# Performance work log

Measured on AMD Instinct MI355X. Metric: run time of the kernel, lower is better.

The kernel has to match this reference:

```python
import jax, jax.numpy as jnp
import numpy as np

B, N, D, H = 2, 2048, 1024, 16
Dh = D // H
SCALE = Dh ** -0.5


def setup_inputs() -> dict:
    key = jax.random.key(0)
    ks = jax.random.split(key, 5)
    init = lambda k, sh, fan: (jax.random.normal(k, sh, jnp.float32) / np.sqrt(fan)).astype(jnp.float32)
    return {
        "x": jax.random.normal(ks[0], (B, N, D), jnp.float32),
        "w_qkv": init(ks[1], (D, 3 * D), D),   # to_qkv (no bias)
        "w_hkv": init(ks[2], (D, 2 * D), D),   # hkv_processor: Linear(dim, 2*dim), split -> HK, HV
        "w_out": init(ks[3], (D, D), D),       # to_out weight
        "b_out": jnp.zeros((D,), jnp.float32), # to_out bias
        "alpha": jnp.ones((1, H, 1, 1), jnp.float32),
    }


def _split_heads(t):  # (B,N,D) -> (B,H,N,Dh)
    return t.reshape(B, N, H, Dh).transpose(0, 2, 1, 3)


def _rope(x, theta=10000.0):
    # lucidrains rotary_embedding_torch: interleaved pairs (x[2i], x[2i+1])
    n, dh = x.shape[-2], x.shape[-1]
    freqs = 1.0 / (theta ** (jnp.arange(0, dh, 2, dtype=jnp.float32) / dh))
    ang = jnp.arange(n, dtype=jnp.float32)[:, None] * freqs          # (N, Dh/2)
    cos = jnp.repeat(jnp.cos(ang), 2, axis=-1)                        # (N, Dh)
    sin = jnp.repeat(jnp.sin(ang), 2, axis=-1)
    xp = x.reshape(*x.shape[:-1], dh // 2, 2)
    xrot = jnp.stack((-xp[..., 1], xp[..., 0]), axis=-1).reshape(x.shape)
    return x * cos + xrot * sin


def reference(x, w_qkv, w_hkv, w_out, b_out, alpha):
    q, k, v = (_split_heads(t) for t in jnp.split(x @ w_qkv, 3, axis=-1))
    hk, hv = (_split_heads(t) for t in jnp.split(x @ w_hkv, 2, axis=-1))
    q = _rope(q)
    k = _rope(k)

    qk = jnp.einsum('bhnd,bhmd->bhnm', q, k) * SCALE          # (B,H,N,N)
    hkk = jnp.einsum('bhnd,bhmd->bhnm', hk, k)                # (B,H,N,N)
    qhk = jnp.sum(q * hk, axis=-1, keepdims=True)             # (B,H,N,1)
    scores = qk - jax.nn.silu(hkk * qhk * SCALE)

    mask = jnp.tril(jnp.ones((N, N), dtype=bool))
    scores = jnp.where(mask, scores, -jnp.inf)
    W = jax.nn.softmax(scores, axis=-1)

    hvv = jnp.einsum('bhnd,bhmd->bhnm', hv, v)                # (B,H,N,N)
    mod = jnp.sum(hvv * W, axis=-1, keepdims=True)            # (B,H,N,1)
    o = jnp.einsum('bhnm,bhmd->bhnd', W, v) - jax.nn.sigmoid(alpha) * mod * hv

    attn_out = o.transpose(0, 2, 1, 3).reshape(B, N, D)
    return attn_out @ w_out + b_out
```

## Files before the change

kernel.cpp:

```cpp
#include <hip/hip_runtime.h>
#include <math.h>

typedef unsigned int u32;
typedef unsigned short u16;
typedef __attribute__((ext_vector_type(4))) float f32x4;
typedef __attribute__((ext_vector_type(8))) short s16x8;

#define BB 2
#define NN 2048
#define DD 1024
#define HH 16
#define ROWS 4096
#define QC 5120
#define SCALE 0.125f
#define LOG2E 1.44269504088896f
#define SC2 (SCALE * LOG2E)

#if __has_builtin(__builtin_amdgcn_exp2f)
#define EXP2(x) __builtin_amdgcn_exp2f(x)
#else
#define EXP2(x) __expf((x) * 0.69314718056f)
#endif
#if __has_builtin(__builtin_amdgcn_rcpf)
#define RCP(x) __builtin_amdgcn_rcpf(x)
#else
#define RCP(x) (1.0f / (x))
#endif

__device__ __forceinline__ u16 f2bf(float x) {
    u32 u = __float_as_uint(x);
    return (u16)((u + 0x7FFFu + ((u >> 16) & 1u)) >> 16);
}
__device__ __forceinline__ float bf2f(u16 h) {
    return __uint_as_float(((u32)h) << 16);
}
__device__ __forceinline__ u32 cvtpk(float lo, float hi) {
    u32 r;
    asm("v_cvt_pk_bf16_f32 %0, %1, %2" : "=v"(r) : "v"(lo), "v"(hi));
    return r;
}
__device__ __forceinline__ void gload16(const void* g, void* l) {
    __builtin_amdgcn_global_load_lds(
        (const __attribute__((address_space(1))) unsigned int*)g,
        (__attribute__((address_space(3))) unsigned int*)l, 16, 0, 0);
}

__device__ __forceinline__ void vt_write(char* vbb, uint4 vreg, int srow, int sch)
{
    uint4 oth;
    oth.x = (u32)__shfl_xor((int)vreg.x, 8); oth.y = (u32)__shfl_xor((int)vreg.y, 8);
    oth.z = (u32)__shfl_xor((int)vreg.z, 8); oth.w = (u32)__shfl_xor((int)vreg.w, 8);
    const bool odd = (srow & 1);
    u32 ma = odd ? vreg.z : vreg.x, mb = odd ? vreg.w : vreg.y;
    u32 oa = odd ? oth.z : oth.x,  ob = odd ? oth.w : oth.y;
    u32 ea = odd ? oa : ma, eb = odd ? ob : mb;
    u32 da = odd ? ma : oa, db = odd ? mb : ob;
    u32 pk0 = (ea & 0xffffu) | (da << 16);
    u32 pk1 = (ea >> 16)     | (da & 0xffff0000u);
    u32 pk2 = (eb & 0xffffu) | (db << 16);
    u32 pk3 = (eb >> 16)     | (db & 0xffff0000u);
    const int s = srow >> 1;
    const int d0 = sch * 8 + (odd ? 4 : 0);
    *(u32*)(vbb + (d0 + 0) * 128 + ((((s >> 2) ^ ((d0 + 0) & 7)) << 4)) + (s & 3) * 4) = pk0;
    *(u32*)(vbb + (d0 + 1) * 128 + ((((s >> 2) ^ ((d0 + 1) & 7)) << 4)) + (s & 3) * 4) = pk1;
    *(u32*)(vbb + (d0 + 2) * 128 + ((((s >> 2) ^ ((d0 + 2) & 7)) << 4)) + (s & 3) * 4) = pk2;
    *(u32*)(vbb + (d0 + 3) * 128 + ((((s >> 2) ^ ((d0 + 3) & 7)) << 4)) + (s & 3) * 4) = pk3;
}

__global__ __launch_bounds__(256) void convert_x(const float* __restrict__ x,
                                                 uint4* __restrict__ xb)
{
    int t = blockIdx.x * 256 + threadIdx.x;
    const float4 a = ((const float4*)x)[2 * t];
    const float4 b = ((const float4*)x)[2 * t + 1];
    uint4 o;
    o.x = f2bf(a.x) | ((u32)f2bf(a.y) << 16);
    o.y = f2bf(a.z) | ((u32)f2bf(a.w) << 16);
    o.z = f2bf(b.x) | ((u32)f2bf(b.y) << 16);
    o.w = f2bf(b.z) | ((u32)f2bf(b.w) << 16);
    xb[t] = o;
}

__global__ __launch_bounds__(256) void transpose_w(const float* __restrict__ wqkv,
                                                   const float* __restrict__ whkv,
                                                   const float* __restrict__ wout,
                                                   u16* __restrict__ wT)
{
    __shared__ float T[64][65];
    const int bc = blockIdx.x;
    const int k0 = blockIdx.y * 64;
    const int c0 = bc * 64;
    const float* src; int stride; int csrc;
    if (bc < 48)      { src = wqkv; stride = 3072; csrc = c0; }
    else if (bc < 80) { src = whkv; stride = 2048; csrc = c0 - 3072; }
    else              { src = wout; stride = 1024; csrc = c0 - 5120; }
    const int t = threadIdx.x;
    const int r = t >> 4, c4 = t & 15;
#pragma unroll
    for (int i = 0; i < 4; ++i) {
        int kk = r + 16 * i;
        float4 v = *(const float4*)&src[(size_t)(k0 + kk) * stride + csrc + 4 * c4];
        T[kk][4 * c4 + 0] = v.x; T[kk][4 * c4 + 1] = v.y;
        T[kk][4 * c4 + 2] = v.z; T[kk][4 * c4 + 3] = v.w;
    }
    __syncthreads();
#pragma unroll
    for (int i = 0; i < 4; ++i) {
        int cc = r + 16 * i;
        u32 lo = f2bf(T[4 * c4 + 0][cc]) | ((u32)f2bf(T[4 * c4 + 1][cc]) << 16);
        u32 hi = f2bf(T[4 * c4 + 2][cc]) | ((u32)f2bf(T[4 * c4 + 3][cc]) << 16);
        *(uint2*)&wT[(size_t)(c0 + cc) * 1024 + k0 + 4 * c4] = make_uint2(lo, hi);
    }
}

__global__ __launch_bounds__(256) void rope_table(float* __restrict__ tab)
{
    int t = blockIdx.x * 256 + threadIdx.x;
    int n = t >> 6, col = t & 63, i = col & 31;
    float ang = (float)n * exp2f(-(float)i * 0.41524101186092029f);
    tab[t] = (col < 32) ? cosf(ang) : sinf(ang);
}

template <int BF16_OUT>
__global__ __launch_bounds__(256, 2) void gemm_bf16(
    const u16* __restrict__ A, int lda,
    const u16* __restrict__ B, int ldb,
    void* __restrict__ C, int ldc,
    const float* __restrict__ bias, const float* __restrict__ tab, int K)
{
    __shared__ u16 As[128 * 64];
    __shared__ u16 Bs[128 * 64];
    const int tid = threadIdx.x;
    const int lane = tid & 63, w = tid >> 6;
    const int g = lane >> 4, c = lane & 15;
    const int wr = w >> 1, wc = w & 1;
    const int rb0 = blockIdx.y * 128, cb0 = blockIdx.x * 128;

    f32x4 acc[4][4];
#pragma unroll
    for (int i = 0; i < 4; ++i)
#pragma unroll
        for (int j = 0; j < 4; ++j) {
            acc[i][j][0] = 0.f; acc[i][j][1] = 0.f; acc[i][j][2] = 0.f; acc[i][j][3] = 0.f;
        }

    const int srow = tid >> 3, sch = tid & 7;
    const int scol = ((sch ^ (srow & 7)) * 8);
    const u16* asrc = A + (size_t)(rb0 + srow) * lda + scol;
    const u16* bsrc = B + (size_t)(cb0 + srow) * ldb + scol;

    for (int k0 = 0; k0 < K; k0 += 64) {
        __syncthreads();
#pragma unroll
        for (int r = 0; r < 4; ++r) {
            gload16(asrc + (size_t)(32 * r) * lda + k0, (char*)As + r * 4096 + w * 1024);
            gload16(bsrc + (size_t)(32 * r) * ldb + k0, (char*)Bs + r * 4096 + w * 1024);
        }
        __syncthreads();
#pragma unroll
        for (int kk = 0; kk < 2; ++kk) {
            s16x8 a[4], b[4];
#pragma unroll
            for (int rb = 0; rb < 4; ++rb) {
                int row = wr * 64 + rb * 16 + c;
                a[rb] = *(const s16x8*)((const char*)As + row * 128 + ((((kk << 2) + g) ^ (row & 7)) << 4));
            }
#pragma unroll
            for (int cb = 0; cb < 4; ++cb) {
                int row = wc * 64 + cb * 16 + c;
                b[cb] = *(const s16x8*)((const char*)Bs + row * 128 + ((((kk << 2) + g) ^ (row & 7)) << 4));
            }
#pragma unroll
            for (int rb = 0; rb < 4; ++rb)
#pragma unroll
                for (int cb = 0; cb < 4; ++cb)
                    acc[rb][cb] = __builtin_amdgcn_mfma_f32_16x16x32_bf16(a[rb], b[cb], acc[rb][cb], 0, 0, 0);
        }
    }

    if (BF16_OUT && tab && cb0 >= 1024 && cb0 < 2048) {
#pragma unroll
        for (int rb = 0; rb < 4; ++rb)
#pragma unroll
            for (int cb = 0; cb < 4; ++cb) {
                const int i = ((wc * 64 + cb * 16 + c) & 63) >> 1;
#pragma unroll
                for (int e = 0; e < 4; ++e) {
                    int n = (rb0 + wr * 64 + rb * 16 + g * 4 + e) & (NN - 1);
                    float co = tab[(n << 6) + i], si = tab[(n << 6) + 32 + i];
                    float self = acc[rb][cb][e];
                    float part = __shfl_xor(self, 1);
                    acc[rb][cb][e] = (c & 1) ? fmaf(self, co, part * si)
                                             : fmaf(self, co, -part * si);
                }
            }
    }

#pragma unroll
    for (int rb = 0; rb < 4; ++rb) {
#pragma unroll
        for (int cb = 0; cb < 4; ++cb) {
            if (BF16_OUT) {
                uint2 keep = make_uint2(0, 0);
#pragma unroll
                for (int e = 0; e < 4; ++e) {
                    u32 me = f2bf(acc[rb][cb][e]);
                    u32 x1 = (u32)__shfl_xor((int)me, 1);
                    u32 pair = (c & 1) ? ((x1 & 0xffffu) | (me << 16)) : ((me & 0xffffu) | (x1 << 16));
                    u32 x2 = (u32)__shfl_xor((int)pair, 2);
                    u32 q0 = (c & 2) ? x2 : pair;
                    u32 q1 = (c & 2) ? pair : x2;
                    if ((c & 3) == e) keep = make_uint2(q0, q1);
                }
                int row = rb0 + wr * 64 + rb * 16 + g * 4 + (c & 3);
                int col = cb0 + wc * 64 + cb * 16 + (c & ~3);
                *(uint2*)((u16*)C + (size_t)row * ldc + col) = keep;
            } else {
                int col = cb0 + wc * 64 + cb * 16 + c;
                float bv = bias ? bias[col] : 0.f;
#pragma unroll
                for (int e = 0; e < 4; ++e) {
                    int row = rb0 + wr * 64 + rb * 16 + g * 4 + e;
                    ((float*)C)[(size_t)row * ldc + col] = acc[rb][cb][e] + bv;
                }
            }
        }
    }
}

__global__ __launch_bounds__(256, 4) void attn(
    const u16* __restrict__ qkvh, const float* __restrict__ alpha,
    const float* __restrict__ tab, u16* __restrict__ aout)
{
    __shared__ u16 Kb[2][64 * 64];
    __shared__ u16 Vt[2][64 * 64];

    const int bid = blockIdx.x;
    const int swz = (bid & 7) * 64 + (bid >> 3);
    const int bh = swz >> 4;
    const int qp = swz & 15;
    const int b = bh >> 4, h = bh & 15;
    const int tid = threadIdx.x;
    const int w = tid >> 6, lane = tid & 63;
    const int g = lane >> 4, c = lane & 15;
    const u16* base = qkvh + (size_t)b * NN * QC;

    const int srow = tid >> 3, sch = tid & 7;
    const int kscol = (sch ^ ((srow & 3) | (((srow >> 3) & 1) << 2))) * 8;
    const u16* ksrc0 = base + (size_t)srow * QC + 1024 + h * 64 + kscol;
    const u16* vsrc0 = base + (size_t)srow * QC + 2048 + h * 64 + sch * 8;

    const float sig_a = RCP(1.f + EXP2(-alpha[h] * LOG2E));
    const int cbase = (8 * (c >> 2) + (c & 3)) * 128;

#pragma unroll 1
    for (int ph = 0; ph < 2; ++ph) {
        const int qt = ph ? (31 - qp) : qp;
        const int q0 = qt * 64;
        const int nrow = q0 + w * 16 + c;

        gload16(ksrc0 + (size_t)(q0 - q0) , (char*)&Kb[0][0] + w * 1024);
        gload16(ksrc0 + (size_t)32 * QC, (char*)&Kb[0][0] + 4096 + w * 1024);
        uint4 vr0 = *(const uint4*)vsrc0;
        uint4 vr1 = *(const uint4*)(vsrc0 + (size_t)32 * QC);
        vt_write((char*)&Vt[0][0], vr0, srow, sch);
        vt_write((char*)&Vt[0][0], vr1, srow + 32, sch);

        s16x8 qf[2], hf[2];
        float qhL;
        {
            const u16* qp_ = base + (size_t)nrow * QC + h * 64;
            float accq = 0.f;
#pragma unroll
            for (int kk = 0; kk < 2; ++kk) {
                uint4 qv = *(const uint4*)(qp_ + ((kk * 4 + g) * 8));
                uint4 hv = *(const uint4*)(qp_ + 3072 + ((kk * 4 + g) * 8));
                const u16* qe = (const u16*)&qv;
                const u16* he = (const u16*)&hv;
                u32 ow[4];
#pragma unroll
                for (int m2 = 0; m2 < 4; ++m2) {
                    int i = (kk * 4 + g) * 4 + m2;
                    float co = tab[(nrow << 6) + i], si = tab[(nrow << 6) + 32 + i];
                    float x0 = bf2f(qe[2 * m2]), x1 = bf2f(qe[2 * m2 + 1]);
                    float r0 = x0 * co - x1 * si;
                    float r1 = x1 * co + x0 * si;
                    accq += r0 * bf2f(he[2 * m2]) + r1 * bf2f(he[2 * m2 + 1]);
                    ow[m2] = (u32)f2bf(r0) | ((u32)f2bf(r1) << 16);
                }
                union { s16x8 v; u32 u[4]; } uq, uh;
                uq.u[0] = ow[0]; uq.u[1] = ow[1]; uq.u[2] = ow[2]; uq.u[3] = ow[3];
                uh.u[0] = hv.x; uh.u[1] = hv.y; uh.u[2] = hv.z; uh.u[3] = hv.w;
                qf[kk] = uq.v; hf[kk] = uh.v;
            }
            accq += __shfl_xor(accq, 16);
            accq += __shfl_xor(accq, 32);
            qhL = accq * SC2;
        }
        __syncthreads();

        f32x4 y[4];
#pragma unroll
        for (int db = 0; db < 4; ++db) { y[db][0] = 0.f; y[db][1] = 0.f; y[db][2] = 0.f; y[db][3] = 0.f; }
        float m = -INFINITY, l = 0.f;

        for (int kt = 0; kt <= qt; ++kt) {
            const int cur = kt & 1;
            const bool haveNext = (kt < qt);
            uint4 vr0n, vr1n;
            if (haveNext) {
                gload16(ksrc0 + (size_t)((kt + 1) * 64) * QC, (char*)&Kb[cur ^ 1][0] + w * 1024);
                gload16(ksrc0 + (size_t)((kt + 1) * 64 + 32) * QC, (char*)&Kb[cur ^ 1][0] + 4096 + w * 1024);
                vr0n = *(const uint4*)(vsrc0 + (size_t)((kt + 1) * 64) * QC);
                vr1n = *(const uint4*)(vsrc0 + (size_t)((kt + 1) * 64 + 32) * QC);
            }

            f32x4 sq[4], sh4[4];
#pragma unroll
            for (int kb = 0; kb < 4; ++kb) {
                sq[kb][0] = 0.f; sq[kb][1] = 0.f; sq[kb][2] = 0.f; sq[kb][3] = 0.f;
                sh4[kb][0] = 0.f; sh4[kb][1] = 0.f; sh4[kb][2] = 0.f; sh4[kb][3] = 0.f;
            }
            const char* kbp = (const char*)&Kb[cur][0] + cbase;
#pragma unroll
            for (int kb = 0; kb < 4; ++kb) {
#pragma unroll
                for (int kk = 0; kk < 2; ++kk) {
                    s16x8 kf = *(const s16x8*)(kbp + (kb & 1) * 512 + (kb >> 1) * 4096 +
                                               ((((kk << 2) + g) ^ (c & 7)) << 4));
                    sq[kb] = __builtin_amdgcn_mfma_f32_16x16x32_bf16(kf, qf[kk], sq[kb], 0, 0, 0);
                    sh4[kb] = __builtin_amdgcn_mfma_f32_16x16x32_bf16(kf, hf[kk], sh4[kb], 0, 0, 0);
                }
            }
            const bool needmask = (kt == qt);
            float mx = -INFINITY;
#pragma unroll
            for (int kb = 0; kb < 4; ++kb) {
#pragma unroll
                for (int e = 0; e < 4; ++e) {
                    float zp = sh4[kb][e] * qhL;
                    float sil = zp * RCP(1.f + EXP2(-zp));
                    float s = fmaf(sq[kb][e], SC2, -sil);
                    if (needmask) {
                        int kg = kt * 64 + 32 * (kb >> 1) + 8 * g + 4 * (kb & 1) + e;
                        if (kg > nrow) s = -INFINITY;
                    }
                    sq[kb][e] = s;
                    mx = fmaxf(mx, s);
                }
            }
            mx = fmaxf(mx, __shfl_xor(mx, 16));
            mx = fmaxf(mx, __shfl_xor(mx, 32));
            const float mnew = fmaxf(m, mx);
            const float scl = EXP2(m - mnew);
            m = mnew;
            float rs = 0.f;
#pragma unroll
            for (int kb = 0; kb < 4; ++kb)
#pragma unroll
                for (int e = 0; e < 4; ++e) {
                    float p = EXP2(sq[kb][e] - mnew);
                    sq[kb][e] = p;
                    rs += p;
                }
            rs += __shfl_xor(rs, 16);
            rs += __shfl_xor(rs, 32);
            l = l * scl + rs;
#pragma unroll
            for (int db = 0; db < 4; ++db) {
                y[db][0] *= scl; y[db][1] *= scl; y[db][2] *= scl; y[db][3] *= scl;
            }
            union { s16x8 v; u32 u[4]; } pa[2];
#pragma unroll
            for (int kk = 0; kk < 2; ++kk) {
                pa[kk].u[0] = cvtpk(sq[2 * kk][0], sq[2 * kk][1]);
                pa[kk].u[1] = cvtpk(sq[2 * kk][2], sq[2 * kk][3]);
                pa[kk].u[2] = cvtpk(sq[2 * kk + 1][0], sq[2 * kk + 1][1]);
                pa[kk].u[3] = cvtpk(sq[2 * kk + 1][2], sq[2 * kk + 1][3]);
            }
            const char* vbp = (const char*)&Vt[cur][0];
#pragma unroll
            for (int kk = 0; kk < 2; ++kk)
#pragma unroll
                for (int db = 0; db < 4; ++db) {
                    int row = db * 16 + c;
                    s16x8 vfr = *(const s16x8*)(vbp + row * 128 + ((((kk << 2) + g) ^ (c & 7)) << 4));
                    y[db] = __builtin_amdgcn_mfma_f32_16x16x32_bf16(vfr, pa[kk].v, y[db], 0, 0, 0);
                }

            if (haveNext) {
                vt_write((char*)&Vt[cur ^ 1][0], vr0n, srow, sch);
                vt_write((char*)&Vt[cur ^ 1][0], vr1n, srow + 32, sch);
            }
            __syncthreads();
        }

        const float inv_l = RCP(l);
        const u16* hvp = base + (size_t)nrow * QC + 4096 + h * 64 + g * 4;
        float hv[4][4];
        float sdot = 0.f;
#pragma unroll
        for (int db = 0; db < 4; ++db) {
            uint2 hw = *(const uint2*)(hvp + db * 16);
            const u16* he = (const u16*)&hw;
#pragma unroll
            for (int e = 0; e < 4; ++e) {
                hv[db][e] = bf2f(he[e]);
                float yn = y[db][e] * inv_l;
                y[db][e] = yn;
                sdot += yn * hv[db][e];
            }
        }
        sdot += __shfl_xor(sdot, 1); sdot += __shfl_xor(sdot, 2);
        sdot += __shfl_xor(sdot, 4); sdot += __shfl_xor(sdot, 8);
        sdot = 0.f;
#pragma unroll
        for (int db = 0; db < 4; ++db)
#pragma unroll
            for (int e = 0; e < 4; ++e) sdot += y[db][e] * hv[db][e];
        sdot += __shfl_xor(sdot, 16);
        sdot += __shfl_xor(sdot, 32);
        const float f = sig_a * sdot;
        u16* op = aout + ((size_t)(b * NN + nrow)) * DD + h * 64 + g * 4;
#pragma unroll
        for (int db = 0; db < 4; ++db) {
            u32 o0 = (u32)f2bf(y[db][0] - f * hv[db][0]) | ((u32)f2bf(y[db][1] - f * hv[db][1]) << 16);
            u32 o1 = (u32)f2bf(y[db][2] - f * hv[db][2]) | ((u32)f2bf(y[db][3] - f * hv[db][3]) << 16);
            *(uint2*)(op + db * 16) = make_uint2(o0, o1);
        }
        __syncthreads();
    }
}

extern "C" void kernel_launch(void* const* d_in, const int* in_sizes, int n_in,
                              void* d_out, int out_size, void* d_ws, size_t ws_size,
                              hipStream_t stream)
{
    const float* x     = (const float*)d_in[0];
    const float* w_qkv = (const float*)d_in[1];
    const float* w_hkv = (const float*)d_in[2];
    const float* w_out = (const float*)d_in[3];
    const float* b_out = (const float*)d_in[4];
    const float* alpha = (const float*)d_in[5];

    char* ws = (char*)d_ws;
    u16*   qkvh = (u16*)ws;
    uint4* xb   = (uint4*)(ws + 41943040);
    u16*   wT   = (u16*)(ws + 50331648);
    u16*   aout = (u16*)(ws + 62914560);
    float* tab  = (float*)(ws + 71303168);

    convert_x<<<2048, 256, 0, stream>>>(x, xb);
    transpose_w<<<dim3(96, 16), 256, 0, stream>>>(w_qkv, w_hkv, w_out, wT);
    rope_table<<<512, 256, 0, stream>>>(tab);

    gemm_bf16<1><<<dim3(40, 32), 256, 0, stream>>>(
        (const u16*)xb, 1024, wT, 1024, qkvh, QC, nullptr, tab, 1024);

    attn<<<512, 256, 0, stream>>>(qkvh, alpha, tab, aout);

    gemm_bf16<0><<<dim3(8, 32), 256, 0, stream>>>(
        aout, 1024, wT + 5120 * 1024, 1024, d_out, 1024, b_out, nullptr, 1024);
}
```

Before: 183.8 us.

## Split paired causal tiles into separate blocks and add V-transpose LDS swizzle

Each attention block used to process a pair of q-tiles (qp and 31-qp) to balance causal work. Now it processes a single q-tile, and the grid doubles to 1024 blocks ordered longest-first so the scheduler can balance the load dynamically. The Vt shared-memory layout gains an extra XOR swizzle term, applied both where it is written and where it is read, to reduce bank conflicts. The change also removes a dead shuffle reduction. The risk is a tail of short blocks and repeated per-block setup.

```diff
diff --git a/kernel.cpp b/kernel.cpp
--- a/kernel.cpp
+++ b/kernel.cpp
@@ -61,10 +61,11 @@
     u32 pk3 = (eb >> 16)     | (db & 0xffff0000u);
     const int s = srow >> 1;
     const int d0 = sch * 8 + (odd ? 4 : 0);
-    *(u32*)(vbb + (d0 + 0) * 128 + ((((s >> 2) ^ ((d0 + 0) & 7)) << 4)) + (s & 3) * 4) = pk0;
-    *(u32*)(vbb + (d0 + 1) * 128 + ((((s >> 2) ^ ((d0 + 1) & 7)) << 4)) + (s & 3) * 4) = pk1;
-    *(u32*)(vbb + (d0 + 2) * 128 + ((((s >> 2) ^ ((d0 + 2) & 7)) << 4)) + (s & 3) * 4) = pk2;
-    *(u32*)(vbb + (d0 + 3) * 128 + ((((s >> 2) ^ ((d0 + 3) & 7)) << 4)) + (s & 3) * 4) = pk3;
+    const int sb = (s & 3) * 4;
+    *(u32*)(vbb + (d0 + 0) * 128 + ((((s >> 2) ^ ((d0 + 0) & 7) ^ sch) << 4)) + sb) = pk0;
+    *(u32*)(vbb + (d0 + 1) * 128 + ((((s >> 2) ^ ((d0 + 1) & 7) ^ sch) << 4)) + sb) = pk1;
+    *(u32*)(vbb + (d0 + 2) * 128 + ((((s >> 2) ^ ((d0 + 2) & 7) ^ sch) << 4)) + sb) = pk2;
+    *(u32*)(vbb + (d0 + 3) * 128 + ((((s >> 2) ^ ((d0 + 3) & 7) ^ sch) << 4)) + sb) = pk3;
 }
 
 __global__ __launch_bounds__(256) void convert_x(const float* __restrict__ x,
@@ -236,14 +237,15 @@
     __shared__ u16 Vt[2][64 * 64];
 
     const int bid = blockIdx.x;
-    const int swz = (bid & 7) * 64 + (bid >> 3);
-    const int bh = swz >> 4;
-    const int qp = swz & 15;
+    const int qt = 31 - (bid >> 5);
+    const int bh = 4 * (bid & 7) + ((bid >> 3) & 3);
     const int b = bh >> 4, h = bh & 15;
     const int tid = threadIdx.x;
     const int w = tid >> 6, lane = tid & 63;
     const int g = lane >> 4, c = lane & 15;
     const u16* base = qkvh + (size_t)b * NN * QC;
+    const int q0 = qt * 64;
+    const int nrow = q0 + w * 16 + c;
 
     const int srow = tid >> 3, sch = tid & 7;
     const int kscol = (sch ^ ((srow & 3) | (((srow >> 3) & 1) << 2))) * 8;
@@ -253,182 +255,168 @@
     const float sig_a = RCP(1.f + EXP2(-alpha[h] * LOG2E));
     const int cbase = (8 * (c >> 2) + (c & 3)) * 128;
 
-#pragma unroll 1
-    for (int ph = 0; ph < 2; ++ph) {
-        const int qt = ph ? (31 - qp) : qp;
-        const int q0 = qt * 64;
-        const int nrow = q0 + w * 16 + c;
-
-        gload16(ksrc0 + (size_t)(q0 - q0) , (char*)&Kb[0][0] + w * 1024);
-        gload16(ksrc0 + (size_t)32 * QC, (char*)&Kb[0][0] + 4096 + w * 1024);
-        uint4 vr0 = *(const uint4*)vsrc0;
-        uint4 vr1 = *(const uint4*)(vsrc0 + (size_t)32 * QC);
-        vt_write((char*)&Vt[0][0], vr0, srow, sch);
-        vt_write((char*)&Vt[0][0], vr1, srow + 32, sch);
-
-        s16x8 qf[2], hf[2];
-        float qhL;
-        {
-            const u16* qp_ = base + (size_t)nrow * QC + h * 64;
-            float accq = 0.f;
+    gload16(ksrc0, (char*)&Kb[0][0] + w * 1024);
+    gload16(ksrc0 + (size_t)32 * QC, (char*)&Kb[0][0] + 4096 + w * 1024);
+    uint4 vr0 = *(const uint4*)vsrc0;
+    uint4 vr1 = *(const uint4*)(vsrc0 + (size_t)32 * QC);
+    vt_write((char*)&Vt[0][0], vr0, srow, sch);
+    vt_write((char*)&Vt[0][0], vr1, srow + 32, sch);
+
+    s16x8 qf[2], hf[2];
+    float qhL;
+    {
+        const u16* qp_ = base + (size_t)nrow * QC + h * 64;
+        float accq = 0.f;
+#pragma unroll
+        for (int kk = 0; kk < 2; ++kk) {
+            uint4 qv = *(const uint4*)(qp_ + ((kk * 4 + g) * 8));
+            uint4 hv = *(const uint4*)(qp_ + 3072 + ((kk * 4 + g) * 8));
+            const u16* qe = (const u16*)&qv;
+            const u16* he = (const u16*)&hv;
+            u32 ow[4];
+#pragma unroll
+            for (int m2 = 0; m2 < 4; ++m2) {
+                int i = (kk * 4 + g) * 4 + m2;
+                float co = tab[(nrow << 6) + i], si = tab[(nrow << 6) + 32 + i];
+                float x0 = bf2f(qe[2 * m2]), x1 = bf2f(qe[2 * m2 + 1]);
+                float r0 = x0 * co - x1 * si;
+                float r1 = x1 * co + x0 * si;
+                accq += r0 * bf2f(he[2 * m2]) + r1 * bf2f(he[2 * m2 + 1]);
+                ow[m2] = (u32)f2bf(r0) | ((u32)f2bf(r1) << 16);
+            }
+            union { s16x8 v; u32 u[4]; } uq, uh;
+            uq.u[0] = ow[0]; uq.u[1] = ow[1]; uq.u[2] = ow[2]; uq.u[3] = ow[3];
+            uh.u[0] = hv.x; uh.u[1] = hv.y; uh.u[2] = hv.z; uh.u[3] = hv.w;
+            qf[kk] = uq.v; hf[kk] = uh.v;
+        }
+        accq += __shfl_xor(accq, 16);
+        accq += __shfl_xor(accq, 32);
+        qhL = accq * SC2;
+    }
+    __syncthreads();
+
+    f32x4 y[4];
+#pragma unroll
+    for (int db = 0; db < 4; ++db) { y[db][0] = 0.f; y[db][1] = 0.f; y[db][2] = 0.f; y[db][3] = 0.f; }
+    float m = -INFINITY, l = 0.f;
+
+    for (int kt = 0; kt <= qt; ++kt) {
+        const int cur = kt & 1;
+        const bool haveNext = (kt < qt);
+        uint4 vr0n, vr1n;
+        if (haveNext) {
+            gload16(ksrc0 + (size_t)((kt + 1) * 64) * QC, (char*)&Kb[cur ^ 1][0] + w * 1024);
+            gload16(ksrc0 + (size_t)((kt + 1) * 64 + 32) * QC, (char*)&Kb[cur ^ 1][0] + 4096 + w * 1024);
+            vr0n = *(const uint4*)(vsrc0 + (size_t)((kt + 1) * 64) * QC);
+            vr1n = *(const uint4*)(vsrc0 + (size_t)((kt + 1) * 64 + 32) * QC);
+        }
+
+        f32x4 sq[4], sh4[4];
+#pragma unroll
+        for (int kb = 0; kb < 4; ++kb) {
+            sq[kb][0] = 0.f; sq[kb][1] = 0.f; sq[kb][2] = 0.f; sq[kb][3] = 0.f;
+            sh4[kb][0] = 0.f; sh4[kb][1] = 0.f; sh4[kb][2] = 0.f; sh4[kb][3] = 0.f;
+        }
+        const char* kbp = (const char*)&Kb[cur][0] + cbase;
+#pragma unroll
+        for (int kb = 0; kb < 4; ++kb) {
 #pragma unroll
             for (int kk = 0; kk < 2; ++kk) {
-                uint4 qv = *(const uint4*)(qp_ + ((kk * 4 + g) * 8));
-                uint4 hv = *(const uint4*)(qp_ + 3072 + ((kk * 4 + g) * 8));
-                const u16* qe = (const u16*)&qv;
-                const u16* he = (const u16*)&hv;
-                u32 ow[4];
-#pragma unroll
-                for (int m2 = 0; m2 < 4; ++m2) {
-                    int i = (kk * 4 + g) * 4 + m2;
-                    float co = tab[(nrow << 6) + i], si = tab[(nrow << 6) + 32 + i];
-                    float x0 = bf2f(qe[2 * m2]), x1 = bf2f(qe[2 * m2 + 1]);
-                    float r0 = x0 * co - x1 * si;
-                    float r1 = x1 * co + x0 * si;
-                    accq += r0 * bf2f(he[2 * m2]) + r1 * bf2f(he[2 * m2 + 1]);
-                    ow[m2] = (u32)f2bf(r0) | ((u32)f2bf(r1) << 16);
+                s16x8 kf = *(const s16x8*)(kbp + (kb & 1) * 512 + (kb >> 1) * 4096 +
+                                           ((((kk << 2) + g) ^ (c & 7)) << 4));
+                sq[kb] = __builtin_amdgcn_mfma_f32_16x16x32_bf16(kf, qf[kk], sq[kb], 0, 0, 0);
+                sh4[kb] = __builtin_amdgcn_mfma_f32_16x16x32_bf16(kf, hf[kk], sh4[kb], 0, 0, 0);
+            }
+        }
+        const bool needmask = (kt == qt);
+        float mx = -INFINITY;
+#pragma unroll
+        for (int kb = 0; kb < 4; ++kb) {
+#pragma unroll
+            for (int e = 0; e < 4; ++e) {
+                float zp = sh4[kb][e] * qhL;
+                float sil = zp * RCP(1.f + EXP2(-zp));
+                float s = fmaf(sq[kb][e], SC2, -sil);
+                if (needmask) {
+                    int kg = kt * 64 + 32 * (kb >> 1) + 8 * g + 4 * (kb & 1) + e;
+                    if (kg > nrow) s = -INFINITY;
                 }
-                union { s16x8 v; u32 u[4]; } uq, uh;
-                uq.u[0] = ow[0]; uq.u[1] = ow[1]; uq.u[2] = ow[2]; uq.u[3] = ow[3];
-                uh.u[0] = hv.x; uh.u[1] = hv.y; uh.u[2] = hv.z; uh.u[3] = hv.w;
-                qf[kk] = uq.v; hf[kk] = uh.v;
-            }
-            accq += __shfl_xor(accq, 16);
-            accq += __shfl_xor(accq, 32);
-            qhL = accq * SC2;
+                sq[kb][e] = s;
+                mx = fmaxf(mx, s);
+            }
+        }
+        mx = fmaxf(mx, __shfl_xor(mx, 16));
+        mx = fmaxf(mx, __shfl_xor(mx, 32));
+        const float mnew = fmaxf(m, mx);
+        const float scl = EXP2(m - mnew);
+        m = mnew;
+        float rs = 0.f;
+#pragma unroll
+        for (int kb = 0; kb < 4; ++kb)
+#pragma unroll
+            for (int e = 0; e < 4; ++e) {
+                float p = EXP2(sq[kb][e] - mnew);
+                sq[kb][e] = p;
+                rs += p;
+            }
+        rs += __shfl_xor(rs, 16);
+        rs += __shfl_xor(rs, 32);
+        l = l * scl + rs;
+#pragma unroll
+        for (int db = 0; db < 4; ++db) {
+            y[db][0] *= scl; y[db][1] *= scl; y[db][2] *= scl; y[db][3] *= scl;
+        }
+        union { s16x8 v; u32 u[4]; } pa[2];
+#pragma unroll
+        for (int kk = 0; kk < 2; ++kk) {
+            pa[kk].u[0] = cvtpk(sq[2 * kk][0], sq[2 * kk][1]);
+            pa[kk].u[1] = cvtpk(sq[2 * kk][2], sq[2 * kk][3]);
+            pa[kk].u[2] = cvtpk(sq[2 * kk + 1][0], sq[2 * kk + 1][1]);
+            pa[kk].u[3] = cvtpk(sq[2 * kk + 1][2], sq[2 * kk + 1][3]);
+        }
+        const char* vbp = (const char*)&Vt[cur][0];
+#pragma unroll
+        for (int kk = 0; kk < 2; ++kk)
+#pragma unroll
+            for (int db = 0; db < 4; ++db) {
+                int row = db * 16 + c;
+                int ch = ((kk << 2) + g) ^ (c & 7) ^ (db * 2 + (c >> 3));
+                s16x8 vfr = *(const s16x8*)(vbp + row * 128 + (ch << 4));
+                y[db] = __builtin_amdgcn_mfma_f32_16x16x32_bf16(vfr, pa[kk].v, y[db], 0, 0, 0);
+            }
+
+        if (haveNext) {
+            vt_write((char*)&Vt[cur ^ 1][0], vr0n, srow, sch);
+            vt_write((char*)&Vt[cur ^ 1][0], vr1n, srow + 32, sch);
         }
         __syncthreads();
-
-        f32x4 y[4];
-#pragma unroll
-        for (int db = 0; db < 4; ++db) { y[db][0] = 0.f; y[db][1] = 0.f; y[db][2] = 0.f; y[db][3] = 0.f; }
-        float m = -INFINITY, l = 0.f;
-
-        for (int kt = 0; kt <= qt; ++kt) {
-            const int cur = kt & 1;
-            const bool haveNext = (kt < qt);
-            uint4 vr0n, vr1n;
-            if (haveNext) {
-                gload16(ksrc0 + (size_t)((kt + 1) * 64) * QC, (char*)&Kb[cur ^ 1][0] + w * 1024);
-                gload16(ksrc0 + (size_t)((kt + 1) * 64 + 32) * QC, (char*)&Kb[cur ^ 1][0] + 4096 + w * 1024);
-                vr0n = *(const uint4*)(vsrc0 + (size_t)((kt + 1) * 64) * QC);
-                vr1n = *(const uint4*)(vsrc0 + (size_t)((kt + 1) * 64 + 32) * QC);
-            }
-
-            f32x4 sq[4], sh4[4];
-#pragma unroll
-            for (int kb = 0; kb < 4; ++kb) {
-                sq[kb][0] = 0.f; sq[kb][1] = 0.f; sq[kb][2] = 0.f; sq[kb][3] = 0.f;
-                sh4[kb][0] = 0.f; sh4[kb][1] = 0.f; sh4[kb][2] = 0.f; sh4[kb][3] = 0.f;
-            }
-            const char* kbp = (const char*)&Kb[cur][0] + cbase;
-#pragma unroll
-            for (int kb = 0; kb < 4; ++kb) {
-#pragma unroll
-                for (int kk = 0; kk < 2; ++kk) {
-                    s16x8 kf = *(const s16x8*)(kbp + (kb & 1) * 512 + (kb >> 1) * 4096 +
-                                               ((((kk << 2) + g) ^ (c & 7)) << 4));
-                    sq[kb] = __builtin_amdgcn_mfma_f32_16x16x32_bf16(kf, qf[kk], sq[kb], 0, 0, 0);
-                    sh4[kb] = __builtin_amdgcn_mfma_f32_16x16x32_bf16(kf, hf[kk], sh4[kb], 0, 0, 0);
-                }
-            }
-            const bool needmask = (kt == qt);
-            float mx = -INFINITY;
-#pragma unroll
-            for (int kb = 0; kb < 4; ++kb) {
-#pragma unroll
-                for (int e = 0; e < 4; ++e) {
-                    float zp = sh4[kb][e] * qhL;
-                    float sil = zp * RCP(1.f + EXP2(-zp));
-                    float s = fmaf(sq[kb][e], SC2, -sil);
-                    if (needmask) {
-                        int kg = kt * 64 + 32 * (kb >> 1) + 8 * g + 4 * (kb & 1) + e;
-                        if (kg > nrow) s = -INFINITY;
-                    }
-                    sq[kb][e] = s;
-                    mx = fmaxf(mx, s);
-                }
-            }
-            mx = fmaxf(mx, __shfl_xor(mx, 16));
-            mx = fmaxf(mx, __shfl_xor(mx, 32));
-            const float mnew = fmaxf(m, mx);
-            const float scl = EXP2(m - mnew);
-            m = mnew;
-            float rs = 0.f;
-#pragma unroll
-            for (int kb = 0; kb < 4; ++kb)
-#pragma unroll
-                for (int e = 0; e < 4; ++e) {
-                    float p = EXP2(sq[kb][e] - mnew);
-                    sq[kb][e] = p;
-                    rs += p;
-                }
-            rs += __shfl_xor(rs, 16);
-            rs += __shfl_xor(rs, 32);
-            l = l * scl + rs;
-#pragma unroll
-            for (int db = 0; db < 4; ++db) {
-                y[db][0] *= scl; y[db][1] *= scl; y[db][2] *= scl; y[db][3] *= scl;
-            }
-            union { s16x8 v; u32 u[4]; } pa[2];
-#pragma unroll
-            for (int kk = 0; kk < 2; ++kk) {
-                pa[kk].u[0] = cvtpk(sq[2 * kk][0], sq[2 * kk][1]);
-                pa[kk].u[1] = cvtpk(sq[2 * kk][2], sq[2 * kk][3]);
-                pa[kk].u[2] = cvtpk(sq[2 * kk + 1][0], sq[2 * kk + 1][1]);
-                pa[kk].u[3] = cvtpk(sq[2 * kk + 1][2], sq[2 * kk + 1][3]);
-            }
-            const char* vbp = (const char*)&Vt[cur][0];
-#pragma unroll
-            for (int kk = 0; kk < 2; ++kk)
-#pragma unroll
-                for (int db = 0; db < 4; ++db) {
-                    int row = db * 16 + c;
-                    s16x8 vfr = *(const s16x8*)(vbp + row * 128 + ((((kk << 2) + g) ^ (c & 7)) << 4));
-                    y[db] = __builtin_amdgcn_mfma_f32_16x16x32_bf16(vfr, pa[kk].v, y[db], 0, 0, 0);
-                }
-
-            if (haveNext) {
-                vt_write((char*)&Vt[cur ^ 1][0], vr0n, srow, sch);
-                vt_write((char*)&Vt[cur ^ 1][0], vr1n, srow + 32, sch);
-            }
-            __syncthreads();
-        }
-
-        const float inv_l = RCP(l);
-        const u16* hvp = base + (size_t)nrow * QC + 4096 + h * 64 + g * 4;
-        float hv[4][4];
-        float sdot = 0.f;
-#pragma unroll
-        for (int db = 0; db < 4; ++db) {
-            uint2 hw = *(const uint2*)(hvp + db * 16);
-            const u16* he = (const u16*)&hw;
-#pragma unroll
-            for (int e = 0; e < 4; ++e) {
-                hv[db][e] = bf2f(he[e]);
-                float yn = y[db][e] * inv_l;
-                y[db][e] = yn;
-                sdot += yn * hv[db][e];
-            }
-        }
-        sdot += __shfl_xor(sdot, 1); sdot += __shfl_xor(sdot, 2);
-        sdot += __shfl_xor(sdot, 4); sdot += __shfl_xor(sdot, 8);
-        sdot = 0.f;
-#pragma unroll
-        for (int db = 0; db < 4; ++db)
-#pragma unroll
-            for (int e = 0; e < 4; ++e) sdot += y[db][e] * hv[db][e];
-        sdot += __shfl_xor(sdot, 16);
-        sdot += __shfl_xor(sdot, 32);
-        const float f = sig_a * sdot;
-        u16* op = aout + ((size_t)(b * NN + nrow)) * DD + h * 64 + g * 4;
-#pragma unroll
-        for (int db = 0; db < 4; ++db) {
-            u32 o0 = (u32)f2bf(y[db][0] - f * hv[db][0]) | ((u32)f2bf(y[db][1] - f * hv[db][1]) << 16);
-            u32 o1 = (u32)f2bf(y[db][2] - f * hv[db][2]) | ((u32)f2bf(y[db][3] - f * hv[db][3]) << 16);
-            *(uint2*)(op + db * 16) = make_uint2(o0, o1);
-        }
-        __syncthreads();
+    }
+
+    const float inv_l = RCP(l);
+    const u16* hvp = base + (size_t)nrow * QC + 4096 + h * 64 + g * 4;
+    float hv[4][4];
+    float sdot = 0.f;
+#pragma unroll
+    for (int db = 0; db < 4; ++db) {
+        uint2 hw = *(const uint2*)(hvp + db * 16);
+        const u16* he = (const u16*)&hw;
+#pragma unroll
+        for (int e = 0; e < 4; ++e) {
+            hv[db][e] = bf2f(he[e]);
+            float yn = y[db][e] * inv_l;
+            y[db][e] = yn;
+            sdot += yn * hv[db][e];
+        }
+    }
+    sdot += __shfl_xor(sdot, 16);
+    sdot += __shfl_xor(sdot, 32);
+    const float f = sig_a * sdot;
+    u16* op = aout + ((size_t)(b * NN + nrow)) * DD + h * 64 + g * 4;
+#pragma unroll
+    for (int db = 0; db < 4; ++db) {
+        u32 o0 = (u32)f2bf(y[db][0] - f * hv[db][0]) | ((u32)f2bf(y[db][1] - f * hv[db][1]) << 16);
+        u32 o1 = (u32)f2bf(y[db][2] - f * hv[db][2]) | ((u32)f2bf(y[db][3] - f * hv[db][3]) << 16);
+        *(uint2*)(op + db * 16) = make_uint2(o0, o1);
     }
 }
 
@@ -457,7 +445,7 @@
     gemm_bf16<1><<<dim3(40, 32), 256, 0, stream>>>(
         (const u16*)xb, 1024, wT, 1024, qkvh, QC, nullptr, tab, 1024);
 
-    attn<<<512, 256, 0, stream>>>(qkvh, alpha, tab, aout);
+    attn<<<1024, 256, 0, stream>>>(qkvh, alpha, tab, aout);
 
     gemm_bf16<0><<<dim3(8, 32), 256, 0, stream>>>(
         aout, 1024, wT + 5120 * 1024, 1024, d_out, 1024, b_out, nullptr, 1024);
```

Result: faster. 168.5 us (-8.4%).
